# Kernel optimization log

Measured on AMD Instinct MI355X. Metric: run time of the kernel, lower is better.

## Reference

```python
import jax, jax.numpy as jnp
import numpy as np

N_NODES = 100000


def gcn_conv(x, edge_index, W, b):
    """PyG GCNConv: symmetric normalization with added self-loops.
    x: [N, Fin], edge_index: [2, E], W: [Fin, Fout], b: [Fout]
    """
    n = x.shape[0]
    h = x @ W  # [N, Fout] dense transform first (standard GCNConv order)
    loops = jnp.arange(n, dtype=edge_index.dtype)
    src = jnp.concatenate([edge_index[0], loops])  # self-loops appended
    dst = jnp.concatenate([edge_index[1], loops])
    deg = jax.ops.segment_sum(jnp.ones_like(dst, dtype=h.dtype), dst, num_segments=n)
    dinv = jax.lax.rsqrt(deg)  # deg >= 1 thanks to self-loops
    norm = dinv[src] * dinv[dst]  # [E+N]
    msgs = h[src] * norm[:, None]  # gather + scale
    out = jax.ops.segment_sum(msgs, dst, num_segments=n)  # scatter-add
    return out + b


def setup_inputs() -> dict:
    key = jax.random.key(0)
    k = jax.random.split(key, 9)
    in_c, hid, out_c = 128, 128, 64
    n_edges = 1600000
    x = jax.random.normal(k[0], (N_NODES, in_c), dtype=jnp.float32)
    edge_index = jax.random.randint(k[1], (2, n_edges), 0, N_NODES, dtype=jnp.int64)
    def lin(kw, kb, fan_in, fan_out):
        bound = 1.0 / np.sqrt(fan_in)
        W = jax.random.uniform(kw, (fan_in, fan_out), jnp.float32, -bound, bound)
        b = jax.random.uniform(kb, (fan_out,), jnp.float32, -bound, bound)
        return W, b
    W1, b1 = lin(k[2], k[3], in_c, hid)
    W2, b2 = lin(k[4], k[5], hid, hid)
    Wf, bf = lin(k[6], k[7], hid, out_c)
    return {"x": x, "edge_index": edge_index, "W1": W1, "b1": b1,
            "W2": W2, "b2": b2, "Wf": Wf, "bf": bf}


def reference(x, edge_index, W1, b1, W2, b2, Wf, bf):
    h = jax.nn.relu(gcn_conv(x, edge_index, W1, b1))
    h = jax.nn.relu(gcn_conv(h, edge_index, W2, b2))
    return h @ Wf + bf
```

## Files before the change

kernel.cpp:

```cpp
#include <hip/hip_runtime.h>
#include <stdint.h>

typedef short short8 __attribute__((ext_vector_type(8)));
typedef float floatx4 __attribute__((ext_vector_type(4)));

#define BK 256

static __device__ __forceinline__ float bflo(unsigned int u) {
    union { unsigned int i; float f; } v; v.i = u << 16; return v.f;
}
static __device__ __forceinline__ float bfhi(unsigned int u) {
    union { unsigned int i; float f; } v; v.i = u & 0xffff0000u; return v.f;
}
static __device__ __forceinline__ unsigned short f2bf(float f) {
    union { float f; unsigned int i; } v; v.f = f;
    unsigned int u = v.i;
    unsigned int r = u + 0x7fffu + ((u >> 16) & 1u);
    return (unsigned short)(r >> 16);
}


__global__ void k_zero_cnt(int* bucket_cnt, int K) {
    int i = blockIdx.x * 256 + threadIdx.x;
    if (i < K) bucket_cnt[i] = 0;
}

__global__ __launch_bounds__(256) void k_hist(const int* __restrict__ dst, int* bucket_cnt,
                                              int E, int N, int K) {
    __shared__ int h[512];
    int t = threadIdx.x;
    for (int i = t; i < K; i += 256) h[i] = 0;
    __syncthreads();
    int per = (E + gridDim.x - 1) / gridDim.x;
    int lo = blockIdx.x * per, hi = min(lo + per, E);
    for (int e = lo + t; e < hi; e += 256) {
        unsigned int d = (unsigned int)dst[e];
        if (d < (unsigned int)N) atomicAdd(&h[d >> 8], 1);
    }
    __syncthreads();
    for (int i = t; i < K; i += 256) if (h[i]) atomicAdd(&bucket_cnt[i], h[i]);
}

__global__ void k_scanK(const int* __restrict__ bucket_cnt, int* bucket_off, int* bucket_cur,
                        int* row_start, int K, int N) {
    __shared__ int s[512];
    int t = threadIdx.x;
    int v = (t < K) ? bucket_cnt[t] : 0;
    s[t] = v; __syncthreads();
    for (int off = 1; off < 512; off <<= 1) {
        int x = (t >= off) ? s[t - off] : 0;
        __syncthreads();
        s[t] += x;
        __syncthreads();
    }
    if (t < K) { bucket_off[t] = s[t] - v; bucket_cur[t] = s[t] - v; }
    if (t == K - 1) { bucket_off[K] = s[t]; row_start[N] = s[t]; }
}

__global__ __launch_bounds__(256) void k_binscatter(const int* __restrict__ src,
                                                    const int* __restrict__ dst,
                                                    int* bucket_cur, uint2* __restrict__ tmp,
                                                    int E, int N, int K) {
    __shared__ int h[512];
    __shared__ int base[512];
    int t = threadIdx.x;
    for (int i = t; i < K; i += 256) h[i] = 0;
    __syncthreads();
    int per = (E + gridDim.x - 1) / gridDim.x;
    int lo = blockIdx.x * per, hi = min(lo + per, E);
    for (int e = lo + t; e < hi; e += 256) {
        unsigned int d = (unsigned int)dst[e], sv = (unsigned int)src[e];
        if (d < (unsigned int)N && sv < (unsigned int)N) atomicAdd(&h[d >> 8], 1);
    }
    __syncthreads();
    for (int i = t; i < K; i += 256) {
        int c = h[i];
        base[i] = c ? atomicAdd(&bucket_cur[i], c) : 0;
        h[i] = 0;
    }
    __syncthreads();
    for (int e = lo + t; e < hi; e += 256) {
        unsigned int d = (unsigned int)dst[e], sv = (unsigned int)src[e];
        if (d < (unsigned int)N && sv < (unsigned int)N) {
            int k = d >> 8;
            int p = base[k] + atomicAdd(&h[k], 1);
            tmp[p] = make_uint2(sv, d);
        }
    }
}

__global__ __launch_bounds__(256) void k_fine(const uint2* __restrict__ tmp,
                                              const int* __restrict__ bucket_off,
                                              int* __restrict__ row_start, float* __restrict__ dinv,
                                              int* __restrict__ csr, int N) {
    __shared__ int deg[BK];
    __shared__ int scn[BK];
    __shared__ int cur[BK];
    int b = blockIdx.x;
    int t = threadIdx.x;
    int lo = bucket_off[b], hi = bucket_off[b + 1];
    deg[t] = 0;
    __syncthreads();
    for (int e = lo + t; e < hi; e += 256) {
        int d = tmp[e].y & (BK - 1);
        atomicAdd(&deg[d], 1);
    }
    __syncthreads();
    int v = deg[t];
    scn[t] = v; __syncthreads();
    for (int off = 1; off < 256; off <<= 1) {
        int x = (t >= off) ? scn[t - off] : 0;
        __syncthreads();
        scn[t] += x;
        __syncthreads();
    }
    int rs = lo + scn[t] - v;
    cur[t] = rs;
    int node = b * BK + t;
    if (node < N) { row_start[node] = rs; dinv[node] = rsqrtf((float)(v + 1)); }
    __syncthreads();
    for (int e = lo + t; e < hi; e += 256) {
        uint2 ed = tmp[e];
        int d = ed.y & (BK - 1);
        int p = atomicAdd(&cur[d], 1);
        csr[p] = (int)ed.x;
    }
}


template <int NOUT, bool SCALE, bool BIAS, bool XF32, bool OUTF32>
__global__ __launch_bounds__(256, 2) void k_gemm(
    const void* __restrict__ Xv, const float* __restrict__ W,
    const float* __restrict__ bias, const float* __restrict__ dinv,
    void* __restrict__ outv, int M) {
    __shared__ __align__(16) unsigned short Wl[NOUT * 136];
    int t = threadIdx.x;
    for (int idx = t; idx < 128 * NOUT; idx += 256) {
        int k = idx / NOUT, n = idx % NOUT;
        Wl[n * 136 + k] = f2bf(W[idx]);
    }
    __syncthreads();

    int wave = t >> 6, lane = t & 63;
    int quad = lane >> 4, l16 = lane & 15;
    int m0 = blockIdx.x * 64 + wave * 16;
    int mr = m0 + l16;
    int mrc = mr < M ? mr : M - 1;

    constexpr int NT = NOUT / 16;
    floatx4 acc[NT];
#pragma unroll
    for (int i = 0; i < NT; i++) acc[i] = (floatx4){0.f, 0.f, 0.f, 0.f};

#pragma unroll
    for (int kc = 0; kc < 4; kc++) {
        short8 a;
        if (XF32) {
            const float* X = (const float*)Xv;
            const float* p = X + (size_t)mrc * 128 + kc * 32 + quad * 8;
            float4 xa = *(const float4*)p;
            float4 xb = *(const float4*)(p + 4);
            a[0] = (short)f2bf(xa.x); a[1] = (short)f2bf(xa.y);
            a[2] = (short)f2bf(xa.z); a[3] = (short)f2bf(xa.w);
            a[4] = (short)f2bf(xb.x); a[5] = (short)f2bf(xb.y);
            a[6] = (short)f2bf(xb.z); a[7] = (short)f2bf(xb.w);
        } else {
            const unsigned short* X = (const unsigned short*)Xv;
            a = *(const short8*)(X + (size_t)mrc * 128 + kc * 32 + quad * 8);
        }
#pragma unroll
        for (int nt = 0; nt < NT; nt++) {
            short8 b = *(const short8*)(&Wl[(nt * 16 + l16) * 136 + kc * 32 + quad * 8]);
            acc[nt] = __builtin_amdgcn_mfma_f32_16x16x32_bf16(a, b, acc[nt], 0, 0, 0);
        }
    }

#pragma unroll
    for (int i = 0; i < 4; i++) {
        int r = m0 + quad * 4 + i;
        if (r >= M) continue;
        float sc = SCALE ? dinv[r] : 1.0f;
#pragma unroll
        for (int nt = 0; nt < NT; nt++) {
            int n = nt * 16 + l16;
            float v = acc[nt][i] * sc;
            if (BIAS) v += bias[n];
            if (OUTF32) {
                ((float*)outv)[(size_t)r * NOUT + n] = v;
            } else {
                ((unsigned short*)outv)[(size_t)r * NOUT + n] = f2bf(v);
            }
        }
    }
}


__global__ __launch_bounds__(256, 4) void k_aggregate(
    const unsigned short* __restrict__ Hs, const int* __restrict__ csr,
    const int* __restrict__ row_start,
    const float* __restrict__ dinv, const float* __restrict__ bias,
    unsigned short* __restrict__ out, int N, int E) {
    int wave = threadIdx.x >> 6, lane = threadIdx.x & 63;
    int node = blockIdx.x * 4 + wave;
    if (node >= N) return;
    int ch = lane * 2;
    int Nm1 = N - 1;

    unsigned int u = *(const unsigned int*)(Hs + (size_t)node * 128 + ch);
    float a0 = bflo(u), a1 = bfhi(u);

    int start = row_start[node];
    int end = row_start[node + 1];
    if (start < 0) start = 0;
    if (end > E) end = E;
    int e = start;
    for (; e + 4 <= end; e += 4) {
        int s0 = min(max(csr[e], 0), Nm1);
        int s1 = min(max(csr[e + 1], 0), Nm1);
        int s2 = min(max(csr[e + 2], 0), Nm1);
        int s3 = min(max(csr[e + 3], 0), Nm1);
        unsigned int u0 = *(const unsigned int*)(Hs + (size_t)s0 * 128 + ch);
        unsigned int u1 = *(const unsigned int*)(Hs + (size_t)s1 * 128 + ch);
        unsigned int u2 = *(const unsigned int*)(Hs + (size_t)s2 * 128 + ch);
        unsigned int u3 = *(const unsigned int*)(Hs + (size_t)s3 * 128 + ch);
        a0 += bflo(u0) + bflo(u1) + bflo(u2) + bflo(u3);
        a1 += bfhi(u0) + bfhi(u1) + bfhi(u2) + bfhi(u3);
    }
    for (; e < end; e++) {
        int s0 = min(max(csr[e], 0), Nm1);
        unsigned int u0 = *(const unsigned int*)(Hs + (size_t)s0 * 128 + ch);
        a0 += bflo(u0);
        a1 += bfhi(u0);
    }

    float di = dinv[node];
    float r0 = fmaxf(fmaf(di, a0, bias[ch]), 0.f);
    float r1 = fmaxf(fmaf(di, a1, bias[ch + 1]), 0.f);
    unsigned int pk = (unsigned int)f2bf(r0) | ((unsigned int)f2bf(r1) << 16);
    *(unsigned int*)(out + (size_t)node * 128 + ch) = pk;
}


extern "C" void kernel_launch(void* const* d_in, const int* in_sizes, int n_in,
                              void* d_out, int out_size, void* d_ws, size_t ws_size,
                              hipStream_t stream) {
    const float* x  = (const float*)d_in[0];
    const int* ei   = (const int*)d_in[1];
    const float* W1 = (const float*)d_in[2];
    const float* b1 = (const float*)d_in[3];
    const float* W2 = (const float*)d_in[4];
    const float* b2 = (const float*)d_in[5];
    const float* Wf = (const float*)d_in[6];
    const float* bf = (const float*)d_in[7];

    int N = in_sizes[0] / 128;
    int E = in_sizes[1] / 2;
    const int* src = ei;
    const int* dst = ei + E;
    int K = (N + BK - 1) / BK;

    size_t need = 0;
    auto pad = [](size_t b) { return (b + 255) & ~(size_t)255; };
    size_t o_bcnt = need; need += pad(512 * 4);
    size_t o_boff = need; need += pad(513 * 4);
    size_t o_bcur = need; need += pad(512 * 4);
    size_t o_rs   = need; need += pad(((size_t)N + 1) * 4);
    size_t o_dinv = need; need += pad((size_t)N * 4);
    size_t o_csr  = need; need += pad((size_t)E * 4);
    size_t o_hs   = need; need += pad((size_t)N * 128 * 2);
    size_t o_a    = need; need += pad((size_t)N * 128 * 2);
    if (ws_size < need) return;
    if ((size_t)E * 8 > (size_t)N * 128 * 2) return;

    char* ws = (char*)d_ws;
    int* bucket_cnt = (int*)(ws + o_bcnt);
    int* bucket_off = (int*)(ws + o_boff);
    int* bucket_cur = (int*)(ws + o_bcur);
    int* row_start  = (int*)(ws + o_rs);
    float* dinv     = (float*)(ws + o_dinv);
    int* csr        = (int*)(ws + o_csr);
    unsigned short* Hs = (unsigned short*)(ws + o_hs);
    unsigned short* A  = (unsigned short*)(ws + o_a);
    uint2* tmp      = (uint2*)A;

    k_zero_cnt<<<(K + 255) / 256, 256, 0, stream>>>(bucket_cnt, K);
    k_hist<<<256, 256, 0, stream>>>(dst, bucket_cnt, E, N, K);
    k_scanK<<<1, 512, 0, stream>>>(bucket_cnt, bucket_off, bucket_cur, row_start, K, N);
    k_binscatter<<<256, 256, 0, stream>>>(src, dst, bucket_cur, tmp, E, N, K);
    k_fine<<<K, 256, 0, stream>>>(tmp, bucket_off, row_start, dinv, csr, N);

    int GB = (N + 63) / 64;
    k_gemm<128, true, false, true, false><<<GB, 256, 0, stream>>>(x, W1, nullptr, dinv, Hs, N);
    k_aggregate<<<(N + 3) / 4, 256, 0, stream>>>(Hs, csr, row_start, dinv, b1, A, N, E);
    k_gemm<128, true, false, false, false><<<GB, 256, 0, stream>>>(A, W2, nullptr, dinv, Hs, N);
    k_aggregate<<<(N + 3) / 4, 256, 0, stream>>>(Hs, csr, row_start, dinv, b2, A, N, E);
    k_gemm<64, false, true, false, true><<<GB, 256, 0, stream>>>(A, Wf, bf, nullptr, d_out, N);
}
```

Baseline: 356.6 us.

## Pre-convert weights to bf16, grid-stride GEMM, deeper unrolled nontemporal aggregation

Adds a kernel that converts each weight matrix to transposed bf16 once, so each GEMM block copies it with vector loads instead of converting per block. GEMM blocks now loop over two row tiles each with a grid-stride loop, halving the grid and the repeated weight staging. The aggregation kernel unrolls the gather to 8 edges, uses nontemporal loads for CSR indices and a nontemporal output store, and raises the launch-bounds occupancy hint. Three extra small launches are added, and the new launch bound may constrain registers.

```diff
diff --git a/kernel.cpp b/kernel.cpp
--- a/kernel.cpp
+++ b/kernel.cpp
@@ -128,74 +128,87 @@
 }
 
 
+__global__ void k_wconv(const float* __restrict__ W, unsigned short* __restrict__ Wt,
+                        int K, int Nc) {
+    int i = blockIdx.x * 256 + threadIdx.x;
+    if (i < K * Nc) {
+        int k = i / Nc, n = i % Nc;
+        Wt[n * K + k] = f2bf(W[i]);
+    }
+}
+
+
 template <int NOUT, bool SCALE, bool BIAS, bool XF32, bool OUTF32>
 __global__ __launch_bounds__(256, 2) void k_gemm(
-    const void* __restrict__ Xv, const float* __restrict__ W,
+    const void* __restrict__ Xv, const unsigned short* __restrict__ Wbf,
     const float* __restrict__ bias, const float* __restrict__ dinv,
-    void* __restrict__ outv, int M) {
+    void* __restrict__ outv, int M, int MB) {
     __shared__ __align__(16) unsigned short Wl[NOUT * 136];
     int t = threadIdx.x;
-    for (int idx = t; idx < 128 * NOUT; idx += 256) {
-        int k = idx / NOUT, n = idx % NOUT;
-        Wl[n * 136 + k] = f2bf(W[idx]);
+    for (int c = t; c < NOUT * 16; c += 256) {
+        short8 v = *(const short8*)(Wbf + (size_t)c * 8);
+        *(short8*)(&Wl[(c >> 4) * 136 + (c & 15) * 8]) = v;
     }
     __syncthreads();
 
     int wave = t >> 6, lane = t & 63;
     int quad = lane >> 4, l16 = lane & 15;
-    int m0 = blockIdx.x * 64 + wave * 16;
-    int mr = m0 + l16;
-    int mrc = mr < M ? mr : M - 1;
-
     constexpr int NT = NOUT / 16;
-    floatx4 acc[NT];
-#pragma unroll
-    for (int i = 0; i < NT; i++) acc[i] = (floatx4){0.f, 0.f, 0.f, 0.f};
-
-#pragma unroll
-    for (int kc = 0; kc < 4; kc++) {
-        short8 a;
-        if (XF32) {
-            const float* X = (const float*)Xv;
-            const float* p = X + (size_t)mrc * 128 + kc * 32 + quad * 8;
-            float4 xa = *(const float4*)p;
-            float4 xb = *(const float4*)(p + 4);
-            a[0] = (short)f2bf(xa.x); a[1] = (short)f2bf(xa.y);
-            a[2] = (short)f2bf(xa.z); a[3] = (short)f2bf(xa.w);
-            a[4] = (short)f2bf(xb.x); a[5] = (short)f2bf(xb.y);
-            a[6] = (short)f2bf(xb.z); a[7] = (short)f2bf(xb.w);
-        } else {
-            const unsigned short* X = (const unsigned short*)Xv;
-            a = *(const short8*)(X + (size_t)mrc * 128 + kc * 32 + quad * 8);
-        }
-#pragma unroll
-        for (int nt = 0; nt < NT; nt++) {
-            short8 b = *(const short8*)(&Wl[(nt * 16 + l16) * 136 + kc * 32 + quad * 8]);
-            acc[nt] = __builtin_amdgcn_mfma_f32_16x16x32_bf16(a, b, acc[nt], 0, 0, 0);
-        }
-    }
-
-#pragma unroll
-    for (int i = 0; i < 4; i++) {
-        int r = m0 + quad * 4 + i;
-        if (r >= M) continue;
-        float sc = SCALE ? dinv[r] : 1.0f;
-#pragma unroll
-        for (int nt = 0; nt < NT; nt++) {
-            int n = nt * 16 + l16;
-            float v = acc[nt][i] * sc;
-            if (BIAS) v += bias[n];
-            if (OUTF32) {
-                ((float*)outv)[(size_t)r * NOUT + n] = v;
+
+    for (int mb = blockIdx.x; mb < MB; mb += gridDim.x) {
+        int m0 = mb * 64 + wave * 16;
+        int mr = m0 + l16;
+        int mrc = mr < M ? mr : M - 1;
+
+        floatx4 acc[NT];
+#pragma unroll
+        for (int i = 0; i < NT; i++) acc[i] = (floatx4){0.f, 0.f, 0.f, 0.f};
+
+#pragma unroll
+        for (int kc = 0; kc < 4; kc++) {
+            short8 a;
+            if (XF32) {
+                const float* X = (const float*)Xv;
+                const float* p = X + (size_t)mrc * 128 + kc * 32 + quad * 8;
+                float4 xa = *(const float4*)p;
+                float4 xb = *(const float4*)(p + 4);
+                a[0] = (short)f2bf(xa.x); a[1] = (short)f2bf(xa.y);
+                a[2] = (short)f2bf(xa.z); a[3] = (short)f2bf(xa.w);
+                a[4] = (short)f2bf(xb.x); a[5] = (short)f2bf(xb.y);
+                a[6] = (short)f2bf(xb.z); a[7] = (short)f2bf(xb.w);
             } else {
-                ((unsigned short*)outv)[(size_t)r * NOUT + n] = f2bf(v);
+                const unsigned short* X = (const unsigned short*)Xv;
+                a = *(const short8*)(X + (size_t)mrc * 128 + kc * 32 + quad * 8);
             }
-        }
-    }
-}
-
-
-__global__ __launch_bounds__(256, 4) void k_aggregate(
+#pragma unroll
+            for (int nt = 0; nt < NT; nt++) {
+                short8 b = *(const short8*)(&Wl[(nt * 16 + l16) * 136 + kc * 32 + quad * 8]);
+                acc[nt] = __builtin_amdgcn_mfma_f32_16x16x32_bf16(a, b, acc[nt], 0, 0, 0);
+            }
+        }
+
+#pragma unroll
+        for (int i = 0; i < 4; i++) {
+            int r = m0 + quad * 4 + i;
+            if (r >= M) continue;
+            float sc = SCALE ? dinv[r] : 1.0f;
+#pragma unroll
+            for (int nt = 0; nt < NT; nt++) {
+                int n = nt * 16 + l16;
+                float v = acc[nt][i] * sc;
+                if (BIAS) v += bias[n];
+                if (OUTF32) {
+                    ((float*)outv)[(size_t)r * NOUT + n] = v;
+                } else {
+                    ((unsigned short*)outv)[(size_t)r * NOUT + n] = f2bf(v);
+                }
+            }
+        }
+    }
+}
+
+
+__global__ __launch_bounds__(256, 8) void k_aggregate(
     const unsigned short* __restrict__ Hs, const int* __restrict__ csr,
     const int* __restrict__ row_start,
     const float* __restrict__ dinv, const float* __restrict__ bias,
@@ -209,26 +222,41 @@
     unsigned int u = *(const unsigned int*)(Hs + (size_t)node * 128 + ch);
     float a0 = bflo(u), a1 = bfhi(u);
 
-    int start = row_start[node];
+    int e = row_start[node];
     int end = row_start[node + 1];
-    if (start < 0) start = 0;
+    if (e < 0) e = 0;
     if (end > E) end = E;
-    int e = start;
-    for (; e + 4 <= end; e += 4) {
-        int s0 = min(max(csr[e], 0), Nm1);
-        int s1 = min(max(csr[e + 1], 0), Nm1);
-        int s2 = min(max(csr[e + 2], 0), Nm1);
-        int s3 = min(max(csr[e + 3], 0), Nm1);
-        unsigned int u0 = *(const unsigned int*)(Hs + (size_t)s0 * 128 + ch);
-        unsigned int u1 = *(const unsigned int*)(Hs + (size_t)s1 * 128 + ch);
-        unsigned int u2 = *(const unsigned int*)(Hs + (size_t)s2 * 128 + ch);
-        unsigned int u3 = *(const unsigned int*)(Hs + (size_t)s3 * 128 + ch);
-        a0 += bflo(u0) + bflo(u1) + bflo(u2) + bflo(u3);
-        a1 += bfhi(u0) + bfhi(u1) + bfhi(u2) + bfhi(u3);
+
+    for (; e + 8 <= end; e += 8) {
+        int idx[8];
+#pragma unroll
+        for (int j = 0; j < 8; j++) idx[j] = __builtin_nontemporal_load(csr + e + j);
+        unsigned int uu[8];
+#pragma unroll
+        for (int j = 0; j < 8; j++) {
+            int s = min(max(idx[j], 0), Nm1);
+            uu[j] = *(const unsigned int*)(Hs + (size_t)s * 128 + ch);
+        }
+#pragma unroll
+        for (int j = 0; j < 8; j++) { a0 += bflo(uu[j]); a1 += bfhi(uu[j]); }
+    }
+    if (e + 4 <= end) {
+        int idx[4];
+#pragma unroll
+        for (int j = 0; j < 4; j++) idx[j] = __builtin_nontemporal_load(csr + e + j);
+        unsigned int uu[4];
+#pragma unroll
+        for (int j = 0; j < 4; j++) {
+            int s = min(max(idx[j], 0), Nm1);
+            uu[j] = *(const unsigned int*)(Hs + (size_t)s * 128 + ch);
+        }
+#pragma unroll
+        for (int j = 0; j < 4; j++) { a0 += bflo(uu[j]); a1 += bfhi(uu[j]); }
+        e += 4;
     }
     for (; e < end; e++) {
-        int s0 = min(max(csr[e], 0), Nm1);
-        unsigned int u0 = *(const unsigned int*)(Hs + (size_t)s0 * 128 + ch);
+        int s = min(max(__builtin_nontemporal_load(csr + e), 0), Nm1);
+        unsigned int u0 = *(const unsigned int*)(Hs + (size_t)s * 128 + ch);
         a0 += bflo(u0);
         a1 += bfhi(u0);
     }
@@ -237,7 +265,7 @@
     float r0 = fmaxf(fmaf(di, a0, bias[ch]), 0.f);
     float r1 = fmaxf(fmaf(di, a1, bias[ch + 1]), 0.f);
     unsigned int pk = (unsigned int)f2bf(r0) | ((unsigned int)f2bf(r1) << 16);
-    *(unsigned int*)(out + (size_t)node * 128 + ch) = pk;
+    __builtin_nontemporal_store(pk, (unsigned int*)(out + (size_t)node * 128 + ch));
 }
 
 
@@ -266,6 +294,7 @@
     size_t o_bcur = need; need += pad(512 * 4);
     size_t o_rs   = need; need += pad(((size_t)N + 1) * 4);
     size_t o_dinv = need; need += pad((size_t)N * 4);
+    size_t o_wbf  = need; need += pad((16384 + 16384 + 8192) * 2);
     size_t o_csr  = need; need += pad((size_t)E * 4);
     size_t o_hs   = need; need += pad((size_t)N * 128 * 2);
     size_t o_a    = need; need += pad((size_t)N * 128 * 2);
@@ -278,10 +307,17 @@
     int* bucket_cur = (int*)(ws + o_bcur);
     int* row_start  = (int*)(ws + o_rs);
     float* dinv     = (float*)(ws + o_dinv);
+    unsigned short* wb1 = (unsigned short*)(ws + o_wbf);
+    unsigned short* wb2 = wb1 + 16384;
+    unsigned short* wbf = wb2 + 16384;
     int* csr        = (int*)(ws + o_csr);
     unsigned short* Hs = (unsigned short*)(ws + o_hs);
     unsigned short* A  = (unsigned short*)(ws + o_a);
     uint2* tmp      = (uint2*)A;
+
+    k_wconv<<<64, 256, 0, stream>>>(W1, wb1, 128, 128);
+    k_wconv<<<64, 256, 0, stream>>>(W2, wb2, 128, 128);
+    k_wconv<<<32, 256, 0, stream>>>(Wf, wbf, 128, 64);
 
     k_zero_cnt<<<(K + 255) / 256, 256, 0, stream>>>(bucket_cnt, K);
     k_hist<<<256, 256, 0, stream>>>(dst, bucket_cnt, E, N, K);
@@ -289,10 +325,12 @@
     k_binscatter<<<256, 256, 0, stream>>>(src, dst, bucket_cur, tmp, E, N, K);
     k_fine<<<K, 256, 0, stream>>>(tmp, bucket_off, row_start, dinv, csr, N);
 
-    int GB = (N + 63) / 64;
-    k_gemm<128, true, false, true, false><<<GB, 256, 0, stream>>>(x, W1, nullptr, dinv, Hs, N);
+    int MB = (N + 63) / 64;
+    int GG = (MB + 1) / 2;
+
+    k_gemm<128, true, false, true, false><<<GG, 256, 0, stream>>>(x, wb1, nullptr, dinv, Hs, N, MB);
     k_aggregate<<<(N + 3) / 4, 256, 0, stream>>>(Hs, csr, row_start, dinv, b1, A, N, E);
-    k_gemm<128, true, false, false, false><<<GB, 256, 0, stream>>>(A, W2, nullptr, dinv, Hs, N);
+    k_gemm<128, true, false, false, false><<<GG, 256, 0, stream>>>(A, wb2, nullptr, dinv, Hs, N, MB);
     k_aggregate<<<(N + 3) / 4, 256, 0, stream>>>(Hs, csr, row_start, dinv, b2, A, N, E);
-    k_gemm<64, false, true, false, true><<<GB, 256, 0, stream>>>(A, Wf, bf, nullptr, d_out, N);
-}
+    k_gemm<64, false, true, false, true><<<GG, 256, 0, stream>>>(A, wbf, bf, nullptr, d_out, N, MB);
+}
```

After: 376.1 us. +5.5%, slower.
